# Kernel optimization log

Hardware: AMD Instinct MI355X
Metric: run time of the kernel (lower is better)

Reference implementation:

```python
import jax, jax.numpy as jnp
import numpy as np
import math

B, H, S, D = 8, 16, 256, 256  # S == D is required by the module's math

def setup_inputs() -> dict:
    key = jax.random.key(0)
    kq, kk, kv, km = jax.random.split(key, 4)
    q = jax.random.normal(kq, (B, H, S, D), dtype=jnp.float32)
    k = jax.random.normal(kk, (B, H, S, D), dtype=jnp.float32)
    v = jax.random.normal(kv, (B, H, S, D), dtype=jnp.float32)
    u = jax.random.uniform(km, (1, H, S, S), dtype=jnp.float32)
    # additive mask: large negative where 'masked', 0.0 elsewhere
    mask = jnp.where(u > 0.7, jnp.float32(-1000.0), jnp.float32(0.0))
    return {"q": q, "k": k, "v": v, "mask": mask}

def reference(q, k, v, mask):
    scale = 1.0 / math.sqrt(q.shape[-1])
    # qk: [B,H,S,S]
    qk = jnp.einsum('bhsd,bhtd->bhst', q, k) * scale + mask
    # first matmul with v: [B,H,S,D] (D == S)
    attn = jnp.einsum('bhst,bhtd->bhsd', qk, v)
    # masked_fill where additive mask == 0.0 (broadcasts [1,H,S,S] -> [B,H,S,D])
    attn = jnp.where(mask == 0.0, jnp.float32(-1e9), attn)
    attn = jax.nn.softmax(attn.astype(jnp.float32), axis=-1).astype(q.dtype)
    # second matmul with v: [B,H,S,D]
    out = jnp.einsum('bhst,bhtd->bhsd', attn, v)
    return out
```

## Files before the change

kernel.cpp:

```cpp
#include <hip/hip_runtime.h>
#include <math.h>

namespace {
constexpr int S  = 256;
constexpr int NT = 256;
constexpr float SCALE = 0.0625f;
constexpr int KLD = 264;
}

typedef __bf16 bf16x4 __attribute__((ext_vector_type(4)));
typedef __bf16 bf16x8 __attribute__((ext_vector_type(8)));
typedef float  f32x4  __attribute__((ext_vector_type(4)));

#define MFMA(a, b, c) __builtin_amdgcn_mfma_f32_16x16x32_bf16((a), (b), (c), 0, 0, 0)

__global__ __launch_bounds__(NT, 2) void prep_kernel(
    const float* __restrict__ q, const float* __restrict__ k,
    const float* __restrict__ v,
    __bf16* __restrict__ vth, __bf16* __restrict__ vtl, __bf16* __restrict__ vtll,
    __bf16* __restrict__ r_hi, __bf16* __restrict__ r_lo,
    int nbh, int swzq)
{
    __shared__ __align__(16) unsigned char lds_arena[64 * KLD * 2 * 2];

    const int tid  = threadIdx.x;
    const int trio = blockIdx.x / 3;
    const int role = blockIdx.x % 3;

    if (role < 2) {
        __bf16* kh = (__bf16*)lds_arena;
        __bf16* kl = kh + 64 * KLD;

        const int w = tid >> 6, l = tid & 63, l15 = l & 15, l4 = l >> 4;

        int L = trio * 2 + role;
        if (swzq) {
            const int n = nbh * 16;
            L = (L & 7) * (n >> 3) + (L >> 3);
        }
        const int bh = L >> 4;
        const int s0 = ((L >> 2) & 3) << 6;
        const int t0 = (L & 3) << 6;

        const float* qb = q + ((size_t)bh << 16);
        const float* kb = k + ((size_t)bh << 16);

        {
            const float* ksrc = kb + (size_t)t0 * S;
            #pragma unroll 4
            for (int it = 0; it < 16; ++it) {
                const int idx = it * 1024 + tid * 4;
                const float4 f = *(const float4*)&ksrc[idx];
                const float xs[4] = {f.x, f.y, f.z, f.w};
                bf16x4 hv, lv;
                #pragma unroll
                for (int e = 0; e < 4; ++e) {
                    const __bf16 hi = (__bf16)xs[e];
                    hv[e] = hi; lv[e] = (__bf16)(xs[e] - (float)hi);
                }
                const int row = idx >> 8;
                const int col = idx & 255;
                *(bf16x4*)&kh[row * KLD + col] = hv;
                *(bf16x4*)&kl[row * KLD + col] = lv;
            }
        }

        bf16x8 qh[8], ql[8];
        {
            const float* qr = qb + (size_t)(s0 + 16 * w + l15) * S;
            #pragma unroll
            for (int kc = 0; kc < 8; ++kc) {
                const float4 f0 = *(const float4*)&qr[kc * 32 + l4 * 8];
                const float4 f1 = *(const float4*)&qr[kc * 32 + l4 * 8 + 4];
                const float xs[8] = {f0.x, f0.y, f0.z, f0.w, f1.x, f1.y, f1.z, f1.w};
                bf16x8 hv, lv;
                #pragma unroll
                for (int e = 0; e < 8; ++e) {
                    const float x = xs[e] * SCALE;
                    const __bf16 hi = (__bf16)x;
                    hv[e] = hi; lv[e] = (__bf16)(x - (float)hi);
                }
                qh[kc] = hv; ql[kc] = lv;
            }
        }
        __syncthreads();

        f32x4 acc[4];
        #pragma unroll
        for (int j = 0; j < 4; ++j) acc[j] = (f32x4){0.f, 0.f, 0.f, 0.f};

        #pragma unroll
        for (int kc = 0; kc < 8; ++kc) {
            #pragma unroll
            for (int j = 0; j < 4; ++j) {
                const int bo = (j * 16 + l15) * KLD + kc * 32 + l4 * 8;
                const bf16x8 khf = *(const bf16x8*)&kh[bo];
                const bf16x8 klf = *(const bf16x8*)&kl[bo];
                acc[j] = MFMA(qh[kc], khf, acc[j]);
                acc[j] = MFMA(qh[kc], klf, acc[j]);
                acc[j] = MFMA(ql[kc], khf, acc[j]);
            }
        }

        __bf16* rh_b = r_hi + ((size_t)bh << 16);
        __bf16* rl_b = r_lo + ((size_t)bh << 16);
        #pragma unroll
        for (int j = 0; j < 4; ++j) {
            #pragma unroll
            for (int rr = 0; rr < 4; ++rr) {
                const int row = s0 + 16 * w + l4 * 4 + rr;
                const int t   = t0 + j * 16 + l15;
                const float rv = acc[j][rr];
                const __bf16 hi = (__bf16)rv;
                rh_b[(size_t)row * S + t] = hi;
                rl_b[(size_t)row * S + t] = (__bf16)(rv - (float)hi);
            }
        }
    } else {
        float (*tile)[257] = (float(*)[257])lds_arena;

        const int vi = trio;
        const int bh = vi >> 3;
        const int tc = vi & 7;

        const float* vb = v + (size_t)bh * S * S + (size_t)tc * 32 * S;
        {
            const int c4 = (tid & 63) * 4;
            const int r  = tid >> 6;
            #pragma unroll
            for (int rr = 0; rr < 8; ++rr) {
                const int row = rr * 4 + r;
                const float4 f = *(const float4*)&vb[(size_t)row * S + c4];
                tile[row][c4 + 0] = f.x; tile[row][c4 + 1] = f.y;
                tile[row][c4 + 2] = f.z; tile[row][c4 + 3] = f.w;
            }
        }
        __syncthreads();

        const size_t obase = (size_t)bh * S * S + (size_t)tc * 8192;
        #pragma unroll
        for (int it = 0; it < 4; ++it) {
            const int id  = it * 256 + tid;
            const int j   = id >> 6;
            const int l4  = (id >> 4) & 3;
            const int l15 = id & 15;
            const int d   = j * 16 + l15;
            const int t0  = l4 * 8;
            bf16x8 hv, lv, llv;
            #pragma unroll
            for (int e = 0; e < 8; ++e) {
                const float x = tile[t0 + e][d];
                const __bf16 hi = (__bf16)x;
                const float  hf = (float)hi;
                const __bf16 lo = (__bf16)(x - hf);
                const float  lf = (float)lo;
                hv[e] = hi; lv[e] = lo; llv[e] = (__bf16)(x - hf - lf);
            }
            const size_t oi = obase + (size_t)id * 8;
            *(bf16x8*)&vth[oi]  = hv;
            *(bf16x8*)&vtl[oi]  = lv;
            *(bf16x8*)&vtll[oi] = llv;
        }
    }
}

#define SRC_OF(sp) ((sp) == 0 ? vth : (sp) == 1 ? vtl : vtll)

#define P2_LOAD(tc)                                                           \
    _Pragma("unroll")                                                         \
    for (int r_ = 0; r_ < 12; ++r_) {                                         \
        const int sp_ = r_ >> 2, qt_ = r_ & 3;                                \
        const __bf16* s_ = SRC_OF(sp_);                                       \
        stg[r_] = *(const bf16x8*)&s_[hb + (size_t)(tc) * 8192 + qt_ * 2048 + tid * 8]; \
    }

#define P2_WRITE()                                                            \
    _Pragma("unroll")                                                         \
    for (int r_ = 0; r_ < 12; ++r_) {                                         \
        const int sp_ = r_ >> 2, qt_ = r_ & 3;                                \
        *(bf16x8*)&arena[sp_ * 8192 + qt_ * 2048 + tid * 8] = stg[r_];        \
    }

#define P3_LOAD(tc)                                                           \
    _Pragma("unroll")                                                         \
    for (int r_ = 0; r_ < 8; ++r_) {                                          \
        const int sp_ = r_ >> 2, qt_ = r_ & 3;                                \
        const __bf16* s_ = SRC_OF(sp_);                                       \
        stg[r_] = *(const bf16x8*)&s_[hb + (size_t)(tc) * 8192 + qt_ * 2048 + tid * 8]; \
    }

#define P3_WRITE()                                                            \
    _Pragma("unroll")                                                         \
    for (int r_ = 0; r_ < 8; ++r_) {                                          \
        const int sp_ = r_ >> 2, qt_ = r_ & 3;                                \
        *(bf16x8*)&arena[16384 + sp_ * 8192 + qt_ * 2048 + tid * 8] = stg[r_];\
    }

__global__ __launch_bounds__(NT, 2) void attn2_kernel(
    const float* __restrict__ mask,
    const __bf16* __restrict__ r_hi, const __bf16* __restrict__ r_lo,
    const __bf16* __restrict__ vth, const __bf16* __restrict__ vtl,
    const __bf16* __restrict__ vtll,
    float* __restrict__ out, int H, int swz)
{
    __shared__ __align__(16) __bf16 arena[32768];

    const int tid = threadIdx.x;
    const int w = tid >> 6, l = tid & 63, l15 = l & 15, l4 = l >> 4;

    int L = blockIdx.x;
    if (swz) L = (blockIdx.x & 7) * ((int)gridDim.x >> 3) + (blockIdx.x >> 3);
    const int bh = L >> 2;
    const int s0 = (L & 3) << 6;
    const int h  = bh % H;

    const size_t hb = (size_t)bh << 16;
    const float* mbase = mask + ((size_t)h << 16);

    const int arow_g = s0 + 16 * w + l15;
    const __bf16* rh_p = r_hi + hb + (size_t)arow_g * S;
    const __bf16* rl_p = r_lo + hb + (size_t)arow_g * S;
    const float*  m_p  = mbase + (size_t)arow_g * S;

    bf16x8 stg[12];

    f32x4 acc2[16];
    #pragma unroll
    for (int j = 0; j < 16; ++j) acc2[j] = (f32x4){0.f, 0.f, 0.f, 0.f};

    P2_LOAD(0);
    P2_WRITE();
    P2_LOAD(1);
    bf16x8 rhc, rlc; float4 m0c, m1c;
    {
        const int ko_ = l4 * 8;
        rhc = *(const bf16x8*)&rh_p[ko_];
        rlc = *(const bf16x8*)&rl_p[ko_];
        m0c = *(const float4*)&m_p[ko_];
        m1c = *(const float4*)&m_p[ko_ + 4];
    }
    __syncthreads();

    #pragma unroll
    for (int tc = 0; tc < 8; ++tc) {
        bf16x8 rhn, rln; float4 m0n, m1n;
        if (tc < 7) {
            const int ko_ = (tc + 1) * 32 + l4 * 8;
            rhn = *(const bf16x8*)&rh_p[ko_];
            rln = *(const bf16x8*)&rl_p[ko_];
            m0n = *(const float4*)&m_p[ko_];
            m1n = *(const float4*)&m_p[ko_ + 4];
        }
        bf16x8 mf;
        mf[0] = (__bf16)m0c.x; mf[1] = (__bf16)m0c.y;
        mf[2] = (__bf16)m0c.z; mf[3] = (__bf16)m0c.w;
        mf[4] = (__bf16)m1c.x; mf[5] = (__bf16)m1c.y;
        mf[6] = (__bf16)m1c.z; mf[7] = (__bf16)m1c.w;

        __builtin_amdgcn_s_setprio(1);
        #pragma unroll
        for (int j = 0; j < 16; ++j) {
            const int fo = j * 512 + l * 8;
            const bf16x8 vh  = *(const bf16x8*)&arena[fo];
            const bf16x8 vl  = *(const bf16x8*)&arena[8192 + fo];
            const bf16x8 vll = *(const bf16x8*)&arena[16384 + fo];
            acc2[j] = MFMA(mf,  vh,  acc2[j]);
            acc2[j] = MFMA(mf,  vl,  acc2[j]);
            acc2[j] = MFMA(mf,  vll, acc2[j]);
            acc2[j] = MFMA(rhc, vh,  acc2[j]);
            acc2[j] = MFMA(rhc, vl,  acc2[j]);
            acc2[j] = MFMA(rlc, vh,  acc2[j]);
        }
        __builtin_amdgcn_s_setprio(0);
        __syncthreads();
        if (tc < 7) {
            P2_WRITE();
            if (tc < 6) P2_LOAD(tc + 2);
            rhc = rhn; rlc = rln; m0c = m0n; m1c = m1n;
            __syncthreads();
        }
    }

    P3_LOAD(0);

    #pragma unroll
    for (int rr = 0; rr < 4; ++rr) {
        const int srow = 16 * w + l4 * 4 + rr;
        const float* mrow = mbase + (size_t)(s0 + srow) * S;
        float mx = -3.4e38f;
        #pragma unroll
        for (int j = 0; j < 16; ++j) {
            const float mval = mrow[j * 16 + l15];
            const float a = (mval == 0.0f) ? -1e9f : acc2[j][rr];
            acc2[j][rr] = a;
            mx = fmaxf(mx, a);
        }
        #pragma unroll
        for (int off = 1; off < 16; off <<= 1)
            mx = fmaxf(mx, __shfl_xor(mx, off, 64));
        float sm = 0.f;
        #pragma unroll
        for (int j = 0; j < 16; ++j) {
            const float e = __expf(acc2[j][rr] - mx);
            acc2[j][rr] = e;
            sm += e;
        }
        #pragma unroll
        for (int off = 1; off < 16; off <<= 1)
            sm += __shfl_xor(sm, off, 64);
        const float inv = 1.0f / sm;
        #pragma unroll
        for (int j = 0; j < 16; ++j) {
            const int t = j * 16 + l15;
            arena[((srow << 8) + t) ^ ((srow & 7) << 3)] = (__bf16)(acc2[j][rr] * inv);
        }
    }
    P3_WRITE();
    P3_LOAD(1);
    __syncthreads();

    f32x4 acc3[16];
    #pragma unroll
    for (int j = 0; j < 16; ++j) acc3[j] = (f32x4){0.f, 0.f, 0.f, 0.f};

    const int prow = 16 * w + l15;
    #pragma unroll
    for (int tc = 0; tc < 8; ++tc) {
        const int pb = ((prow << 8) + tc * 32 + l4 * 8) ^ ((prow & 7) << 3);
        const bf16x8 pa = *(const bf16x8*)&arena[pb];
        __builtin_amdgcn_s_setprio(1);
        #pragma unroll
        for (int j = 0; j < 16; ++j) {
            const int fo = 16384 + j * 512 + l * 8;
            acc3[j] = MFMA(pa, *(const bf16x8*)&arena[fo], acc3[j]);
            acc3[j] = MFMA(pa, *(const bf16x8*)&arena[8192 + fo], acc3[j]);
        }
        __builtin_amdgcn_s_setprio(0);
        __syncthreads();
        if (tc < 7) {
            P3_WRITE();
            if (tc < 6) P3_LOAD(tc + 2);
            __syncthreads();
        }
    }

    float* ob = out + hb + (size_t)s0 * S;
    #pragma unroll
    for (int j = 0; j < 16; ++j) {
        #pragma unroll
        for (int rr = 0; rr < 4; ++rr)
            ob[(size_t)(16 * w + l4 * 4 + rr) * S + j * 16 + l15] = acc3[j][rr];
    }
}

__global__ __launch_bounds__(NT) void transpose_k_kernel(
    const float* __restrict__ k, float* __restrict__ kt)
{
    __shared__ float tile[64][65];
    const int tileIdx = blockIdx.x & 15;
    const int bh      = blockIdx.x >> 4;
    const int ti = (tileIdx >> 2) * 64;
    const int tj = (tileIdx & 3) * 64;
    const float* kb = k  + (size_t)bh * S * S;
    float*      ktb = kt + (size_t)bh * S * S;
    const int c  = threadIdx.x & 63;
    const int r4 = threadIdx.x >> 6;
    #pragma unroll
    for (int rr = 0; rr < 64; rr += 4)
        tile[rr + r4][c] = kb[(size_t)(ti + rr + r4) * S + tj + c];
    __syncthreads();
    #pragma unroll
    for (int rr = 0; rr < 64; rr += 4)
        ktb[(size_t)(tj + rr + r4) * S + ti + c] = tile[c][rr + r4];
}

template <int RPB>
__global__ __launch_bounds__(NT) void fused_attn_rpb(
    const float* __restrict__ q, const float* __restrict__ kt,
    const float* __restrict__ v, const float* __restrict__ mask,
    float* __restrict__ out, int nbh, int H, int swizzle)
{
    __shared__ float qT[S][RPB];
    __shared__ float sT[S][RPB];
    __shared__ float redbuf[4][RPB];

    const int tid = threadIdx.x;
    constexpr int NRB = S / RPB;
    int bh, rb;
    if (swizzle) {
        const int xcd  = blockIdx.x & 7;
        const int slot = blockIdx.x >> 3;
        const int hpx  = nbh >> 3;
        bh = xcd * hpx + (slot % hpx);
        rb = slot / hpx;
    } else {
        bh = blockIdx.x / NRB;
        rb = blockIdx.x % NRB;
    }
    const int h  = bh % H;
    const int s0 = rb * RPB;

    const float* qb  = q    + (size_t)bh * S * S;
    const float* ktb = kt   + (size_t)bh * S * S;
    const float* vb  = v    + (size_t)bh * S * S;
    const float* mb  = mask + (size_t)h  * S * S + (size_t)s0 * S;
    float*       ob  = out  + (size_t)bh * S * S + (size_t)s0 * S;

    #pragma unroll
    for (int si = 0; si < RPB; ++si)
        qT[tid][si] = qb[(size_t)(s0 + si) * S + tid];
    __syncthreads();

    {
        float acc[RPB];
        #pragma unroll
        for (int si = 0; si < RPB; ++si) acc[si] = 0.f;
        #pragma unroll 4
        for (int i = 0; i < S; ++i) {
            const float kv = ktb[(size_t)i * S + tid];
            #pragma unroll
            for (int si4 = 0; si4 < RPB; si4 += 4) {
                const float4 qa = *reinterpret_cast<const float4*>(&qT[i][si4]);
                acc[si4+0] = fmaf(qa.x, kv, acc[si4+0]);
                acc[si4+1] = fmaf(qa.y, kv, acc[si4+1]);
                acc[si4+2] = fmaf(qa.z, kv, acc[si4+2]);
                acc[si4+3] = fmaf(qa.w, kv, acc[si4+3]);
            }
        }
        #pragma unroll
        for (int si4 = 0; si4 < RPB; si4 += 4) {
            float4 t4;
            t4.x = fmaf(acc[si4+0], SCALE, mb[(size_t)(si4+0)*S + tid]);
            t4.y = fmaf(acc[si4+1], SCALE, mb[(size_t)(si4+1)*S + tid]);
            t4.z = fmaf(acc[si4+2], SCALE, mb[(size_t)(si4+2)*S + tid]);
            t4.w = fmaf(acc[si4+3], SCALE, mb[(size_t)(si4+3)*S + tid]);
            *reinterpret_cast<float4*>(&sT[tid][si4]) = t4;
        }
    }
    __syncthreads();

    float a1[RPB];
    #pragma unroll
    for (int si = 0; si < RPB; ++si) a1[si] = 0.f;
    #pragma unroll 2
    for (int t = 0; t < S; ++t) {
        const float vv = vb[(size_t)t * S + tid];
        #pragma unroll
        for (int si4 = 0; si4 < RPB; si4 += 4) {
            const float4 pa = *reinterpret_cast<const float4*>(&sT[t][si4]);
            a1[si4+0] = fmaf(pa.x, vv, a1[si4+0]);
            a1[si4+1] = fmaf(pa.y, vv, a1[si4+1]);
            a1[si4+2] = fmaf(pa.z, vv, a1[si4+2]);
            a1[si4+3] = fmaf(pa.w, vv, a1[si4+3]);
        }
    }
    #pragma unroll
    for (int si = 0; si < RPB; ++si)
        if (mb[(size_t)si * S + tid] == 0.0f) a1[si] = -1e9f;

    const int lane = tid & 63;
    const int wv   = tid >> 6;
    #pragma unroll
    for (int si = 0; si < RPB; ++si) {
        float m = a1[si];
        #pragma unroll
        for (int off = 32; off > 0; off >>= 1)
            m = fmaxf(m, __shfl_down(m, off, 64));
        if (lane == 0) redbuf[wv][si] = m;
    }
    __syncthreads();
    float e[RPB];
    #pragma unroll
    for (int si = 0; si < RPB; ++si) {
        const float m = fmaxf(fmaxf(redbuf[0][si], redbuf[1][si]),
                              fmaxf(redbuf[2][si], redbuf[3][si]));
        e[si] = __expf(a1[si] - m);
    }
    __syncthreads();
    #pragma unroll
    for (int si = 0; si < RPB; ++si) {
        float sm = e[si];
        #pragma unroll
        for (int off = 32; off > 0; off >>= 1)
            sm += __shfl_down(sm, off, 64);
        if (lane == 0) redbuf[wv][si] = sm;
    }
    __syncthreads();
    #pragma unroll
    for (int si4 = 0; si4 < RPB; si4 += 4) {
        float4 t4;
        #pragma unroll
        for (int jj = 0; jj < 4; ++jj) {
            const int si = si4 + jj;
            const float sm = redbuf[0][si] + redbuf[1][si] +
                             redbuf[2][si] + redbuf[3][si];
            (&t4.x)[jj] = e[si] / sm;
        }
        *reinterpret_cast<float4*>(&sT[tid][si4]) = t4;
    }
    __syncthreads();

    float o[RPB];
    #pragma unroll
    for (int si = 0; si < RPB; ++si) o[si] = 0.f;
    #pragma unroll 2
    for (int t = 0; t < S; ++t) {
        const float vv = vb[(size_t)t * S + tid];
        #pragma unroll
        for (int si4 = 0; si4 < RPB; si4 += 4) {
            const float4 pa = *reinterpret_cast<const float4*>(&sT[t][si4]);
            o[si4+0] = fmaf(pa.x, vv, o[si4+0]);
            o[si4+1] = fmaf(pa.y, vv, o[si4+1]);
            o[si4+2] = fmaf(pa.z, vv, o[si4+2]);
            o[si4+3] = fmaf(pa.w, vv, o[si4+3]);
        }
    }
    #pragma unroll
    for (int si = 0; si < RPB; ++si)
        ob[(size_t)si * S + tid] = o[si];
}

extern "C" void kernel_launch(void* const* d_in, const int* in_sizes, int n_in,
                              void* d_out, int out_size, void* d_ws, size_t ws_size,
                              hipStream_t stream) {
    const float* q    = (const float*)d_in[0];
    const float* k    = (const float*)d_in[1];
    const float* v    = (const float*)d_in[2];
    const float* mask = (const float*)d_in[3];
    float* out = (float*)d_out;

    const int nbh = in_sizes[0] / (S * S);
    const int H   = in_sizes[3] / (S * S);
    const size_t he = (size_t)nbh * S * S;
    const size_t need = he * sizeof(__bf16) * 5;
    const size_t kt_bytes = he * sizeof(float);

    if (ws_size >= need) {
        __bf16* vth  = (__bf16*)d_ws;
        __bf16* vtl  = vth + he;
        __bf16* vtll = vtl + he;
        __bf16* rhi  = vtll + he;
        __bf16* rlo  = rhi + he;
        const int nblk_q = nbh * 16;
        const int nblk_a = nbh * 4;
        const int swzq = (nblk_q % 8 == 0) ? 1 : 0;
        const int swza = (nblk_a % 8 == 0) ? 1 : 0;
        prep_kernel<<<dim3(nbh * 24), NT, 0, stream>>>(
            q, k, v, vth, vtl, vtll, rhi, rlo, nbh, swzq);
        attn2_kernel<<<dim3(nblk_a), NT, 0, stream>>>(
            mask, rhi, rlo, vth, vtl, vtll, out, H, swza);
    } else if (ws_size >= kt_bytes) {
        float* kt = (float*)d_ws;
        transpose_k_kernel<<<dim3(nbh * 16), NT, 0, stream>>>(k, kt);
        constexpr int RPB = 16;
        const int grid = nbh * (S / RPB);
        const int swz = (nbh % 8 == 0) ? 1 : 0;
        fused_attn_rpb<RPB><<<dim3(grid), NT, 0, stream>>>(
            q, kt, v, mask, out, nbh, H, swz);
    }
}
```

Measured before the change: 85.73 us.

## Shrink QK tiles, restage R through LDS in fragment layout, raise prep occupancy

The QK prep blocks now cover 64x32 output tiles instead of 64x64, so there are four QK blocks per V-transpose block and launch_bounds allows four blocks per CU. The R hi/lo results are staged through LDS and written to global in the MFMA fragment order that attn2 consumes. Each lane now issues one contiguous 16-byte store instead of scattered 2-byte stores, and attn2 reads its A fragments contiguously. The trade-off is twice as many Q-row loads and bf16 splits across blocks, an extra LDS round trip and barrier, and the Q swizzle is now always on.

```diff
diff --git a/kernel.cpp b/kernel.cpp
--- a/kernel.cpp
+++ b/kernel.cpp
@@ -14,33 +14,33 @@
 
 #define MFMA(a, b, c) __builtin_amdgcn_mfma_f32_16x16x32_bf16((a), (b), (c), 0, 0, 0)
 
-__global__ __launch_bounds__(NT, 2) void prep_kernel(
+__global__ __launch_bounds__(NT, 4) void prep_kernel(
     const float* __restrict__ q, const float* __restrict__ k,
     const float* __restrict__ v,
     __bf16* __restrict__ vth, __bf16* __restrict__ vtl, __bf16* __restrict__ vtll,
     __bf16* __restrict__ r_hi, __bf16* __restrict__ r_lo,
     int nbh, int swzq)
 {
-    __shared__ __align__(16) unsigned char lds_arena[64 * KLD * 2 * 2];
+    __shared__ __align__(16) unsigned char lds_arena[32 * KLD * 2 * 2];
 
     const int tid  = threadIdx.x;
-    const int trio = blockIdx.x / 3;
-    const int role = blockIdx.x % 3;
-
-    if (role < 2) {
+    const int grp  = blockIdx.x / 5;
+    const int role = blockIdx.x % 5;
+
+    if (role < 4) {
         __bf16* kh = (__bf16*)lds_arena;
-        __bf16* kl = kh + 64 * KLD;
+        __bf16* kl = kh + 32 * KLD;
 
         const int w = tid >> 6, l = tid & 63, l15 = l & 15, l4 = l >> 4;
 
-        int L = trio * 2 + role;
+        int L = grp * 4 + role;
         if (swzq) {
-            const int n = nbh * 16;
+            const int n = nbh * 32;
             L = (L & 7) * (n >> 3) + (L >> 3);
         }
-        const int bh = L >> 4;
-        const int s0 = ((L >> 2) & 3) << 6;
-        const int t0 = (L & 3) << 6;
+        const int bh = L >> 5;
+        const int s0 = ((L >> 3) & 3) << 6;
+        const int t0 = (L & 7) << 5;
 
         const float* qb = q + ((size_t)bh << 16);
         const float* kb = k + ((size_t)bh << 16);
@@ -48,7 +48,7 @@
         {
             const float* ksrc = kb + (size_t)t0 * S;
             #pragma unroll 4
-            for (int it = 0; it < 16; ++it) {
+            for (int it = 0; it < 8; ++it) {
                 const int idx = it * 1024 + tid * 4;
                 const float4 f = *(const float4*)&ksrc[idx];
                 const float xs[4] = {f.x, f.y, f.z, f.w};
@@ -85,14 +85,14 @@
         }
         __syncthreads();
 
-        f32x4 acc[4];
-        #pragma unroll
-        for (int j = 0; j < 4; ++j) acc[j] = (f32x4){0.f, 0.f, 0.f, 0.f};
+        f32x4 acc[2];
+        acc[0] = (f32x4){0.f, 0.f, 0.f, 0.f};
+        acc[1] = (f32x4){0.f, 0.f, 0.f, 0.f};
 
         #pragma unroll
         for (int kc = 0; kc < 8; ++kc) {
             #pragma unroll
-            for (int j = 0; j < 4; ++j) {
+            for (int j = 0; j < 2; ++j) {
                 const int bo = (j * 16 + l15) * KLD + kc * 32 + l4 * 8;
                 const bf16x8 khf = *(const bf16x8*)&kh[bo];
                 const bf16x8 klf = *(const bf16x8*)&kl[bo];
@@ -101,25 +101,33 @@
                 acc[j] = MFMA(ql[kc], khf, acc[j]);
             }
         }
-
-        __bf16* rh_b = r_hi + ((size_t)bh << 16);
-        __bf16* rl_b = r_lo + ((size_t)bh << 16);
-        #pragma unroll
-        for (int j = 0; j < 4; ++j) {
+        __syncthreads();
+
+        __bf16* rb = kh;
+        #pragma unroll
+        for (int j = 0; j < 2; ++j) {
             #pragma unroll
             for (int rr = 0; rr < 4; ++rr) {
-                const int row = s0 + 16 * w + l4 * 4 + rr;
-                const int t   = t0 + j * 16 + l15;
                 const float rv = acc[j][rr];
                 const __bf16 hi = (__bf16)rv;
-                rh_b[(size_t)row * S + t] = hi;
-                rl_b[(size_t)row * S + t] = (__bf16)(rv - (float)hi);
-            }
-        }
+                const __bf16 lo = (__bf16)(rv - (float)hi);
+                const int elem = ((l4 * 4 + rr) + 16 * (2 * j + (l15 >> 3))) * 8
+                               + (l15 & 7);
+                rb[w * 1024 + elem]       = hi;
+                rb[w * 1024 + 512 + elem] = lo;
+            }
+        }
+        const int sb = (s0 >> 4) + w;
+        const int tc = t0 >> 5;
+        const size_t hb = (size_t)bh << 16;
+        const bf16x8 ph = *(const bf16x8*)&rb[w * 1024 + l * 8];
+        const bf16x8 pl = *(const bf16x8*)&rb[w * 1024 + 512 + l * 8];
+        *(bf16x8*)&r_hi[hb + (size_t)sb * 4096 + (size_t)tc * 512 + l * 8] = ph;
+        *(bf16x8*)&r_lo[hb + (size_t)sb * 4096 + (size_t)tc * 512 + l * 8] = pl;
     } else {
         float (*tile)[257] = (float(*)[257])lds_arena;
 
-        const int vi = trio;
+        const int vi = grp;
         const int bh = vi >> 3;
         const int tc = vi & 7;
 
@@ -217,10 +225,10 @@
     const size_t hb = (size_t)bh << 16;
     const float* mbase = mask + ((size_t)h << 16);
 
-    const int arow_g = s0 + 16 * w + l15;
-    const __bf16* rh_p = r_hi + hb + (size_t)arow_g * S;
-    const __bf16* rl_p = r_lo + hb + (size_t)arow_g * S;
-    const float*  m_p  = mbase + (size_t)arow_g * S;
+    const int sb_a = (s0 >> 4) + w;
+    const __bf16* rh_p = r_hi + hb + (size_t)sb_a * 4096;
+    const __bf16* rl_p = r_lo + hb + (size_t)sb_a * 4096;
+    const float*  m_p  = mbase + (size_t)(s0 + 16 * w + l15) * S;
 
     bf16x8 stg[12];
 
@@ -233,11 +241,10 @@
     P2_LOAD(1);
     bf16x8 rhc, rlc; float4 m0c, m1c;
     {
-        const int ko_ = l4 * 8;
-        rhc = *(const bf16x8*)&rh_p[ko_];
-        rlc = *(const bf16x8*)&rl_p[ko_];
-        m0c = *(const float4*)&m_p[ko_];
-        m1c = *(const float4*)&m_p[ko_ + 4];
+        rhc = *(const bf16x8*)&rh_p[l * 8];
+        rlc = *(const bf16x8*)&rl_p[l * 8];
+        m0c = *(const float4*)&m_p[l4 * 8];
+        m1c = *(const float4*)&m_p[l4 * 8 + 4];
     }
     __syncthreads();
 
@@ -245,9 +252,9 @@
     for (int tc = 0; tc < 8; ++tc) {
         bf16x8 rhn, rln; float4 m0n, m1n;
         if (tc < 7) {
+            rhn = *(const bf16x8*)&rh_p[(tc + 1) * 512 + l * 8];
+            rln = *(const bf16x8*)&rl_p[(tc + 1) * 512 + l * 8];
             const int ko_ = (tc + 1) * 32 + l4 * 8;
-            rhn = *(const bf16x8*)&rh_p[ko_];
-            rln = *(const bf16x8*)&rl_p[ko_];
             m0n = *(const float4*)&m_p[ko_];
             m1n = *(const float4*)&m_p[ko_ + 4];
         }
@@ -541,12 +548,10 @@
         __bf16* vtll = vtl + he;
         __bf16* rhi  = vtll + he;
         __bf16* rlo  = rhi + he;
-        const int nblk_q = nbh * 16;
         const int nblk_a = nbh * 4;
-        const int swzq = (nblk_q % 8 == 0) ? 1 : 0;
         const int swza = (nblk_a % 8 == 0) ? 1 : 0;
-        prep_kernel<<<dim3(nbh * 24), NT, 0, stream>>>(
-            q, k, v, vth, vtl, vtll, rhi, rlo, nbh, swzq);
+        prep_kernel<<<dim3(nbh * 40), NT, 0, stream>>>(
+            q, k, v, vth, vtl, vtll, rhi, rlo, nbh, 1);
         attn2_kernel<<<dim3(nblk_a), NT, 0, stream>>>(
             mask, rhi, rlo, vth, vtl, vtll, out, H, swza);
     } else if (ws_size >= kt_bytes) {
```

Result: slower. 91.98 us (+7.3%).
